# Optimization experiments

Measured on AMD Instinct MI355X. Metric: run time of the kernel, lower is better.

Reference implementation:

```python
import jax, jax.numpy as jnp
import numpy as np

BN_EPS = 1e-5

def _conv1x1(x, W, b):
    # x: [B,C,H,W], W: [O,C], b: [O]
    return jnp.einsum('bchw,oc->bohw', x, W) + b[None, :, None, None]

def setup_inputs() -> dict:
    key = jax.random.key(0)
    ks = jax.random.split(key, 9)
    B, C, H, W = 8, 256, 64, 64
    Ci = C // 2
    s_in = 0.05  # small init scale to keep softmax well-conditioned
    return {
        'x': jax.random.normal(ks[0], (B, C, H, W), jnp.float32),
        'theta_w': jax.random.normal(ks[1], (Ci, C), jnp.float32) * s_in,
        'theta_b': jnp.zeros((Ci,), jnp.float32),
        'phi_w': jax.random.normal(ks[2], (Ci, C), jnp.float32) * s_in,
        'phi_b': jnp.zeros((Ci,), jnp.float32),
        'g_w': jax.random.normal(ks[3], (Ci, C), jnp.float32) * s_in,
        'g_b': jnp.zeros((Ci,), jnp.float32),
        'out_w': jax.random.normal(ks[4], (C, Ci), jnp.float32) * s_in,
        'out_b': jnp.zeros((C,), jnp.float32),
        'gamma': jnp.ones((C,), jnp.float32),
        'beta': jnp.zeros((C,), jnp.float32),
    }

def reference(x, theta_w, theta_b, phi_w, phi_b, g_w, g_b, out_w, out_b, gamma, beta):
    B, C, H, W = x.shape
    Ci = C // 2
    N = H * W
    theta = _conv1x1(x, theta_w, theta_b).reshape(B, Ci, N)  # [B,Ci,N]
    phi = _conv1x1(x, phi_w, phi_b).reshape(B, Ci, N)        # [B,Ci,N]
    g = _conv1x1(x, g_w, g_b).reshape(B, Ci, N)              # [B,Ci,N]
    scale = 1.0 / jnp.sqrt(jnp.asarray(Ci, x.dtype))
    sim = jnp.einsum('bcn,bcm->bnm', theta, phi) * scale     # [B,N,N]
    attn = jax.nn.softmax(sim, axis=-1)
    y = jnp.einsum('bnm,bcm->bcn', attn, g).reshape(B, Ci, H, W)
    y = _conv1x1(y, out_w, out_b)                            # [B,C,H,W]
    # BatchNorm2d, training-mode statistics (biased variance), as in torch default
    mean = y.mean(axis=(0, 2, 3))
    var = y.var(axis=(0, 2, 3))
    y = (y - mean[None, :, None, None]) * jax.lax.rsqrt(var + BN_EPS)[None, :, None, None]
    y = y * gamma[None, :, None, None] + beta[None, :, None, None]
    return x + y
```

## Files before the change

### kernel.cpp

```cpp
#include <hip/hip_runtime.h>
#include <hip/hip_bf16.h>

typedef __bf16 bf16x8 __attribute__((ext_vector_type(8)));
typedef float f32x4 __attribute__((ext_vector_type(4)));
typedef float f32x16 __attribute__((ext_vector_type(16)));

#define B_ 8
#define C_ 256
#define CI 128
#define N_ 4096

__device__ __forceinline__ float exp2fast(float x) {
    return __builtin_amdgcn_exp2f(x);
}
__device__ __forceinline__ ushort f2bf(float f) {
    union { float f; unsigned u; } v; v.f = f;
    unsigned r = v.u + 0x7fffu + ((v.u >> 16) & 1u);
    return (ushort)(r >> 16);
}
__device__ __forceinline__ float bf2f(ushort u) {
    union { unsigned u; float f; } v; v.u = ((unsigned)u) << 16;
    return v.f;
}
__device__ __forceinline__ unsigned cvtpk(float lo, float hi) {
    unsigned r;
    asm("v_cvt_pk_bf16_f32 %0, %1, %2" : "=v"(r) : "v"(lo), "v"(hi));
    return r;
}
__device__ __forceinline__ void plswap(unsigned& a, unsigned& b) {
    asm volatile("v_permlane32_swap_b32 %0, %1" : "+v"(a), "+v"(b));
}
__device__ __forceinline__ void gld16(const void* src, void* dst) {
    __builtin_amdgcn_global_load_lds(
        (const __attribute__((address_space(1))) unsigned*)src,
        (__attribute__((address_space(3))) unsigned*)dst, 16, 0, 0);
}

__global__ void k_prep(const float* __restrict__ tw, const float* __restrict__ pw,
                       const float* __restrict__ gw, const float* __restrict__ ow,
                       ushort* __restrict__ wbf, ushort* __restrict__ owbf) {
    int idx = blockIdx.x * 256 + threadIdx.x;
    if (idx < 384 * 256) {
        int i = idx >> 8, c = idx & 255;
        float v = (i < 128) ? tw[i * 256 + c]
                : (i < 256) ? pw[(i - 128) * 256 + c]
                            : gw[(i - 256) * 256 + c];
        wbf[idx] = f2bf(v);
    }
    if (idx < 256 * 128) owbf[idx] = f2bf(ow[idx]);
}

__global__ __launch_bounds__(256) void k_transpose(const float* __restrict__ x,
                                                   ushort* __restrict__ xt) {
    __shared__ __align__(16) float tile[64][65];
    int b = blockIdx.z, c0 = blockIdx.y * 64, n0 = blockIdx.x * 64;
    int t = threadIdx.x;
    int cl = t >> 2, nc = (t & 3) * 16;
    const float* src = x + ((size_t)(b * 256 + c0 + cl)) * N_ + n0 + nc;
#pragma unroll
    for (int j = 0; j < 4; j++) {
        float4 v = *reinterpret_cast<const float4*>(src + 4 * j);
        tile[cl][nc + 4 * j + 0] = v.x;
        tile[cl][nc + 4 * j + 1] = v.y;
        tile[cl][nc + 4 * j + 2] = v.z;
        tile[cl][nc + 4 * j + 3] = v.w;
    }
    __syncthreads();
    int nl = t >> 2, cc = (t & 3) * 16;
    ushort* dst = xt + ((size_t)b * N_ + n0 + nl) * 256 + c0 + cc;
#pragma unroll
    for (int j = 0; j < 4; j++) {
        ushort4 o;
        o.x = f2bf(tile[cc + 4 * j + 0][nl]);
        o.y = f2bf(tile[cc + 4 * j + 1][nl]);
        o.z = f2bf(tile[cc + 4 * j + 2][nl]);
        o.w = f2bf(tile[cc + 4 * j + 3][nl]);
        *reinterpret_cast<ushort4*>(dst + 4 * j) = o;
    }
}

__global__ __launch_bounds__(256) void k_qkv(const ushort* __restrict__ wbf,
                                             const ushort* __restrict__ xt,
                                             const float* __restrict__ tb,
                                             const float* __restrict__ pb,
                                             const float* __restrict__ gb,
                                             ushort* __restrict__ qt,
                                             ushort* __restrict__ kt,
                                             ushort* __restrict__ gv) {
    __shared__ __align__(16) ushort lt[4][64][72];
    int nt = blockIdx.x, it = blockIdx.y, b = blockIdx.z;
    int tid = threadIdx.x, w = tid >> 6, l = tid & 63, lr = l & 15, lg = l >> 4;
    int i_off = it * 128 + (w >> 1) * 64;
    int n_off = nt * 128 + (w & 1) * 64;
    const ushort* xb = xt + (size_t)b * N_ * 256;

    f32x4 acc[4][4];
#pragma unroll
    for (int i = 0; i < 4; i++)
#pragma unroll
        for (int j = 0; j < 4; j++) acc[i][j] = (f32x4)0.0f;

#pragma unroll
    for (int kc = 0; kc < 8; kc++) {
        int ko = kc * 32 + lg * 8;
        bf16x8 a[4], bb[4];
#pragma unroll
        for (int fi = 0; fi < 4; fi++)
            a[fi] = *reinterpret_cast<const bf16x8*>(wbf + (size_t)(i_off + fi * 16 + lr) * 256 + ko);
#pragma unroll
        for (int fn = 0; fn < 4; fn++)
            bb[fn] = *reinterpret_cast<const bf16x8*>(xb + (size_t)(n_off + fn * 16 + lr) * 256 + ko);
#pragma unroll
        for (int fi = 0; fi < 4; fi++)
#pragma unroll
            for (int fn = 0; fn < 4; fn++)
                acc[fi][fn] = __builtin_amdgcn_mfma_f32_16x16x32_bf16(a[fi], bb[fn], acc[fi][fn], 0, 0, 0);
    }

    const float* bias = (it == 0) ? tb : (it == 1) ? pb : gb;
    const float mul = (it == 0) ? (0.08838834764831845f * 1.4426950408889634f) : 1.0f;
    if (it == 2) {
        char* g = (char*)(gv + (size_t)b * CI * N_);
#pragma unroll
        for (int fi = 0; fi < 4; fi++)
#pragma unroll
            for (int reg = 0; reg < 4; reg++) {
                int cl = (w >> 1) * 64 + fi * 16 + lg * 4 + reg;
                float bv = bias[cl];
                int cbyte = (cl & 7) * 16 + (cl >> 3) * 512;
#pragma unroll
                for (int fn = 0; fn < 4; fn++) {
                    int n = n_off + fn * 16 + lr;
                    size_t byte = (size_t)(n >> 5) * 8192 + cbyte
                                + ((n >> 3) & 3) * 128 + (n & 7) * 2;
                    *(ushort*)(g + byte) = f2bf(acc[fi][fn][reg] + bv);
                }
            }
    } else {
#pragma unroll
        for (int fi = 0; fi < 4; fi++)
#pragma unroll
            for (int reg = 0; reg < 4; reg++) {
                int il = fi * 16 + lg * 4 + reg;
                float bv = bias[(w >> 1) * 64 + il];
#pragma unroll
                for (int fn = 0; fn < 4; fn++)
                    lt[w][fn * 16 + lr][il] = f2bf((acc[fi][fn][reg] + bv) * mul);
            }
        __builtin_amdgcn_s_waitcnt(0);
        ushort* dst = ((it == 0) ? qt : kt) + (size_t)b * N_ * CI;
        ushort* drow = dst + (size_t)(n_off + l) * CI + (w >> 1) * 64;
#pragma unroll
        for (int cc = 0; cc < 8; cc++) {
            uint4 v = *reinterpret_cast<uint4*>(&lt[w][l][cc * 8]);
            *reinterpret_cast<uint4*>(drow + cc * 8) = v;
        }
    }
}

__global__ __launch_bounds__(256, 2) void k_attn(const ushort* __restrict__ qt,
                                                 const ushort* __restrict__ kt,
                                                 const ushort* __restrict__ gv,
                                                 ushort* __restrict__ yt) {
    __shared__ __align__(16) char smem[65536];
    int bid = blockIdx.x;
    int b = bid & 7, qb = bid >> 3;
    int tid = threadIdx.x, w = tid >> 6, l = tid & 63;
    int p = w >> 1, s = w & 1;
    int l31 = l & 31, lh = l >> 5;
    const ushort* qtb = qt + (size_t)b * N_ * CI;
    const ushort* ktb = kt + (size_t)b * N_ * CI;
    const ushort* gvb = gv + (size_t)b * CI * N_;
    char* kbuf = smem + p * 16384;
    char* vbuf = smem + 32768 + p * 16384;
    const int pbase = p * 2048;
    const int nq = qb * 64 + s * 32;
    const int q = nq + l31;
    const int swk = (l31 & 7) << 4;
    const int vrb = (l31 & 7) * 16 + lh * 128 + (l31 >> 3) * 512;

    bf16x8 qf[8];
#pragma unroll
    for (int kc = 0; kc < 8; kc++)
        qf[kc] = *reinterpret_cast<const bf16x8*>(qtb + (size_t)q * CI + kc * 16 + lh * 8);

    f32x16 acc[4];
#pragma unroll
    for (int fc = 0; fc < 4; fc++) acc[fc] = (f32x16)0.0f;
    float lrun = 0.f;

#define STAGE(t_, bi)                                                              \
    do {                                                                           \
        int m0_ = pbase + (t_) * 32;                                               \
        const char* ks_ = (const char*)(ktb + (size_t)m0_ * CI);                   \
        const char* vs_ = (const char*)gvb + (size_t)m0_ * 256;                    \
        char* kd_ = kbuf + (bi) * 8192;                                            \
        char* vd_ = vbuf + (bi) * 8192;                                            \
        _Pragma("unroll")                                                          \
        for (int i_ = 0; i_ < 4; ++i_) {                                           \
            int cc = i_ * 128 + s * 64 + l;                                        \
            int m_ = cc >> 4, hb = (cc & 15) << 4;                                 \
            gld16(ks_ + m_ * 256 + (hb ^ ((m_ & 7) << 4)), kd_ + cc * 16);         \
        }                                                                          \
        _Pragma("unroll")                                                          \
        for (int i_ = 0; i_ < 4; ++i_) {                                           \
            int cc = i_ * 128 + s * 64 + l;                                        \
            gld16(vs_ + cc * 16, vd_ + cc * 16);                                   \
        }                                                                          \
    } while (0)

    STAGE(0, 0);
    __syncthreads();

    for (int t = 0; t < 64; ++t) {
        int cur = t & 1;
        if (t < 63) STAGE(t + 1, cur ^ 1);
        const char* kbc = kbuf + cur * 8192;
        const char* vbc = vbuf + cur * 8192;

        f32x16 Sa = (f32x16)0.0f, Sb = (f32x16)0.0f;
        __builtin_amdgcn_s_setprio(1);
#pragma unroll
        for (int kc = 0; kc < 8; kc += 2) {
            bf16x8 kf0 = *reinterpret_cast<const bf16x8*>(
                kbc + l31 * 256 + ((kc * 32 + lh * 16) ^ swk));
            bf16x8 kf1 = *reinterpret_cast<const bf16x8*>(
                kbc + l31 * 256 + (((kc + 1) * 32 + lh * 16) ^ swk));
            Sa = __builtin_amdgcn_mfma_f32_32x32x16_bf16(kf0, qf[kc], Sa, 0, 0, 0);
            Sb = __builtin_amdgcn_mfma_f32_32x32x16_bf16(kf1, qf[kc + 1], Sb, 0, 0, 0);
        }
        __builtin_amdgcn_s_setprio(0);

        float pv[16];
        float rs = 0.f;
#pragma unroll
        for (int r = 0; r < 16; r++) {
            pv[r] = exp2fast(Sa[r] + Sb[r]);
            rs += pv[r];
        }
        lrun += rs;

        unsigned u0 = cvtpk(pv[0], pv[1]),  u1 = cvtpk(pv[2], pv[3]);
        unsigned u2 = cvtpk(pv[4], pv[5]),  u3 = cvtpk(pv[6], pv[7]);
        unsigned u4 = cvtpk(pv[8], pv[9]),  u5 = cvtpk(pv[10], pv[11]);
        unsigned u6 = cvtpk(pv[12], pv[13]), u7 = cvtpk(pv[14], pv[15]);
        plswap(u0, u2);
        plswap(u1, u3);
        plswap(u4, u6);
        plswap(u5, u7);
        union { unsigned u[4]; bf16x8 v; } pb0, pb1;
        pb0.u[0] = u0; pb0.u[1] = u1; pb0.u[2] = u2; pb0.u[3] = u3;
        pb1.u[0] = u4; pb1.u[1] = u5; pb1.u[2] = u6; pb1.u[3] = u7;

        __builtin_amdgcn_s_setprio(1);
#pragma unroll
        for (int mk = 0; mk < 2; mk++) {
            bf16x8 pf = mk ? pb1.v : pb0.v;
#pragma unroll
            for (int fc = 0; fc < 4; fc++) {
                bf16x8 vf = *reinterpret_cast<const bf16x8*>(vbc + vrb + mk * 256 + fc * 2048);
                acc[fc] = __builtin_amdgcn_mfma_f32_32x32x16_bf16(vf, pf, acc[fc], 0, 0, 0);
            }
        }
        __builtin_amdgcn_s_setprio(0);
        __syncthreads();
    }
#undef STAGE

    lrun += __shfl_xor(lrun, 32);

    float* accb = (float*)smem;
    float* mlb = (float*)(smem + 34816);
    if (p == 0) {
        float* ab = accb + s * (64 * 68) + l * 68;
#pragma unroll
        for (int fc = 0; fc < 4; fc++)
            *reinterpret_cast<f32x16*>(ab + fc * 16) = acc[fc];
        if (l < 32) mlb[s * 32 + l] = lrun;
    }
    __syncthreads();
    if (p == 1) {
        float l0 = mlb[s * 32 + l31];
        float inv = 1.f / (lrun + l0);
        const float* ab = accb + s * (64 * 68) + l * 68;
        ushort* yb = yt + (size_t)b * N_ * CI + (size_t)q * CI;
#pragma unroll
        for (int fc = 0; fc < 4; fc++) {
            f32x16 a0 = *reinterpret_cast<const f32x16*>(ab + fc * 16);
#pragma unroll
            for (int rg = 0; rg < 4; rg++) {
                ushort4 o;
                o.x = f2bf((acc[fc][rg * 4 + 0] + a0[rg * 4 + 0]) * inv);
                o.y = f2bf((acc[fc][rg * 4 + 1] + a0[rg * 4 + 1]) * inv);
                o.z = f2bf((acc[fc][rg * 4 + 2] + a0[rg * 4 + 2]) * inv);
                o.w = f2bf((acc[fc][rg * 4 + 3] + a0[rg * 4 + 3]) * inv);
                *reinterpret_cast<ushort4*>(yb + fc * 32 + rg * 8 + lh * 4) = o;
            }
        }
    }
}

__global__ __launch_bounds__(256) void k_outconv(const ushort* __restrict__ owbf,
                                                 const ushort* __restrict__ yt,
                                                 const float* __restrict__ ob,
                                                 ushort* __restrict__ pre,
                                                 float* __restrict__ part) {
    int nt = blockIdx.x, ot = blockIdx.y, b = blockIdx.z;
    int tid = threadIdx.x, w = tid >> 6, l = tid & 63, lr = l & 15, lg = l >> 4;
    int o_off = ot * 128 + (w >> 1) * 64;
    int n_off = nt * 128 + (w & 1) * 64;
    const ushort* yb = yt + (size_t)b * N_ * CI;

    f32x4 acc[4][4];
#pragma unroll
    for (int i = 0; i < 4; i++)
#pragma unroll
        for (int j = 0; j < 4; j++) acc[i][j] = (f32x4)0.0f;

#pragma unroll
    for (int kc = 0; kc < 4; kc++) {
        int ko = kc * 32 + lg * 8;
        bf16x8 a[4], bb[4];
#pragma unroll
        for (int fo = 0; fo < 4; fo++)
            a[fo] = *reinterpret_cast<const bf16x8*>(owbf + (size_t)(o_off + fo * 16 + lr) * CI + ko);
#pragma unroll
        for (int fn = 0; fn < 4; fn++)
            bb[fn] = *reinterpret_cast<const bf16x8*>(yb + (size_t)(n_off + fn * 16 + lr) * CI + ko);
#pragma unroll
        for (int fo = 0; fo < 4; fo++)
#pragma unroll
            for (int fn = 0; fn < 4; fn++)
                acc[fo][fn] = __builtin_amdgcn_mfma_f32_16x16x32_bf16(a[fo], bb[fn], acc[fo][fn], 0, 0, 0);
    }

    ushort* pb_ = pre + (size_t)b * C_ * N_;
#pragma unroll
    for (int fo = 0; fo < 4; fo++)
#pragma unroll
        for (int reg = 0; reg < 4; reg++) {
            int o = o_off + fo * 16 + lg * 4 + reg;
            float bv = ob[o];
            float s1 = 0.f, s2 = 0.f;
#pragma unroll
            for (int fn = 0; fn < 4; fn++) {
                float v = acc[fo][fn][reg] + bv;
                pb_[(size_t)o * N_ + n_off + fn * 16 + lr] = f2bf(v);
                s1 += v;
                s2 += v * v;
            }
#pragma unroll
            for (int d = 1; d < 16; d <<= 1) {
                s1 += __shfl_xor(s1, d);
                s2 += __shfl_xor(s2, d);
            }
            if (lr == 0) {
                int slot = (b * 32 + nt) * 2 + (w & 1);
                part[((size_t)o * 512 + slot) * 2 + 0] = s1;
                part[((size_t)o * 512 + slot) * 2 + 1] = s2;
            }
        }
}

__global__ void k_stats(const float* __restrict__ part, const float* __restrict__ gamma,
                        const float* __restrict__ beta, float* __restrict__ stats) {
    int o = blockIdx.x, t = threadIdx.x;
    __shared__ float r1[256], r2[256];
    float s1 = part[((size_t)o * 512 + t) * 2 + 0] + part[((size_t)o * 512 + t + 256) * 2 + 0];
    float s2 = part[((size_t)o * 512 + t) * 2 + 1] + part[((size_t)o * 512 + t + 256) * 2 + 1];
    r1[t] = s1; r2[t] = s2;
    __syncthreads();
    for (int s = 128; s > 0; s >>= 1) {
        if (t < s) { r1[t] += r1[t + s]; r2[t] += r2[t + s]; }
        __syncthreads();
    }
    if (t == 0) {
        float cnt = 1.f / (float)(B_ * N_);
        float mean = r1[0] * cnt;
        float var = r2[0] * cnt - mean * mean;
        float inv = rsqrtf(var + 1e-5f);
        float a = gamma[o] * inv;
        stats[o * 2 + 0] = a;
        stats[o * 2 + 1] = beta[o] - mean * a;
    }
}

__global__ void k_final(const float* __restrict__ x, const ushort* __restrict__ pre,
                        const float* __restrict__ stats, float* __restrict__ out) {
    int idx = blockIdx.x * 256 + threadIdx.x;
    int o = (idx >> 10) & 255;
    float a = stats[o * 2 + 0], c = stats[o * 2 + 1];
    float4 xv = reinterpret_cast<const float4*>(x)[idx];
    ushort4 pv = reinterpret_cast<const ushort4*>(pre)[idx];
    float4 ov;
    ov.x = xv.x + bf2f(pv.x) * a + c;
    ov.y = xv.y + bf2f(pv.y) * a + c;
    ov.z = xv.z + bf2f(pv.z) * a + c;
    ov.w = xv.w + bf2f(pv.w) * a + c;
    reinterpret_cast<float4*>(out)[idx] = ov;
}

extern "C" void kernel_launch(void* const* d_in, const int* in_sizes, int n_in,
                              void* d_out, int out_size, void* d_ws, size_t ws_size,
                              hipStream_t stream) {
    const float* x  = (const float*)d_in[0];
    const float* tw = (const float*)d_in[1];
    const float* tb = (const float*)d_in[2];
    const float* pw = (const float*)d_in[3];
    const float* pb = (const float*)d_in[4];
    const float* gw = (const float*)d_in[5];
    const float* gb = (const float*)d_in[6];
    const float* ow = (const float*)d_in[7];
    const float* ob = (const float*)d_in[8];
    const float* gamma = (const float*)d_in[9];
    const float* beta  = (const float*)d_in[10];

    char* ws = (char*)d_ws;
    const size_t WBF_OFF  = 0;
    const size_t OWBF_OFF = WBF_OFF + 196608;
    const size_t XT_OFF   = OWBF_OFF + 65536;
    const size_t QT_OFF   = XT_OFF + 16777216;
    const size_t KT_OFF   = QT_OFF + 8388608;
    const size_t GV_OFF   = KT_OFF + 8388608;
    const size_t YT_OFF   = GV_OFF + 8388608;
    const size_t PRE_OFF  = YT_OFF + 8388608;
    const size_t PART_OFF = PRE_OFF + 16777216;
    const size_t ST_OFF   = PART_OFF + 1048576;

    ushort* wbf  = (ushort*)(ws + WBF_OFF);
    ushort* owbf = (ushort*)(ws + OWBF_OFF);
    ushort* xt   = (ushort*)(ws + XT_OFF);
    ushort* qt   = (ushort*)(ws + QT_OFF);
    ushort* kt   = (ushort*)(ws + KT_OFF);
    ushort* gv   = (ushort*)(ws + GV_OFF);
    ushort* yt   = (ushort*)(ws + YT_OFF);
    ushort* pre  = (ushort*)(ws + PRE_OFF);
    float*  part = (float*)(ws + PART_OFF);
    float*  stats= (float*)(ws + ST_OFF);

    k_prep<<<384, 256, 0, stream>>>(tw, pw, gw, ow, wbf, owbf);
    k_transpose<<<dim3(64, 4, 8), 256, 0, stream>>>(x, xt);
    k_qkv<<<dim3(32, 3, 8), 256, 0, stream>>>(wbf, xt, tb, pb, gb, qt, kt, gv);
    k_attn<<<512, 256, 0, stream>>>(qt, kt, gv, yt);
    k_outconv<<<dim3(32, 2, 8), 256, 0, stream>>>(owbf, yt, ob, pre, part);
    k_stats<<<256, 256, 0, stream>>>(part, gamma, beta, stats);
    k_final<<<8192, 256, 0, stream>>>(x, pre, stats, (float*)d_out);
}
```

Measured before the change: 168.2 us.

## Widen attention blocks to 1024 threads with four-way KV split and shared tiles

The attention kernel now runs 256 blocks of 16 waves instead of 512 blocks of 4 waves. Each block handles 128 queries with four KV partitions of 1024 keys, so each staged K/V tile is reused by four query-slice waves instead of two. The cross-partition reduction now goes through LDS in two rounds, with partition 0 summing the partials and the row sums. LDS use doubles to 128KB per block, and the higher wave count per SIMD tightens the register budget, which risks spills given the 64-float accumulators plus the Q fragments.

Measured after the change: 264.7 us. +57.4%, slower.

```diff
diff --git a/kernel.cpp b/kernel.cpp
--- a/kernel.cpp
+++ b/kernel.cpp
@@ -158,26 +158,27 @@
     }
 }
 
-__global__ __launch_bounds__(256, 2) void k_attn(const ushort* __restrict__ qt,
-                                                 const ushort* __restrict__ kt,
-                                                 const ushort* __restrict__ gv,
-                                                 ushort* __restrict__ yt) {
-    __shared__ __align__(16) char smem[65536];
+__global__ __launch_bounds__(1024, 4) void k_attn(const ushort* __restrict__ qt,
+                                                  const ushort* __restrict__ kt,
+                                                  const ushort* __restrict__ gv,
+                                                  ushort* __restrict__ yt) {
+    __shared__ __align__(16) char smem[131072];
     int bid = blockIdx.x;
     int b = bid & 7, qb = bid >> 3;
     int tid = threadIdx.x, w = tid >> 6, l = tid & 63;
-    int p = w >> 1, s = w & 1;
+    int p = w >> 2, s = w & 3;
     int l31 = l & 31, lh = l >> 5;
     const ushort* qtb = qt + (size_t)b * N_ * CI;
     const ushort* ktb = kt + (size_t)b * N_ * CI;
     const ushort* gvb = gv + (size_t)b * CI * N_;
     char* kbuf = smem + p * 16384;
-    char* vbuf = smem + 32768 + p * 16384;
-    const int pbase = p * 2048;
-    const int nq = qb * 64 + s * 32;
+    char* vbuf = smem + 65536 + p * 16384;
+    const int pbase = p * 1024;
+    const int nq = qb * 128 + s * 32;
     const int q = nq + l31;
     const int swk = (l31 & 7) << 4;
     const int vrb = (l31 & 7) * 16 + lh * 128 + (l31 >> 3) * 512;
+    const int ls = s * 64 + l;
 
     bf16x8 qf[8];
 #pragma unroll
@@ -197,14 +198,14 @@
         char* kd_ = kbuf + (bi) * 8192;                                            \
         char* vd_ = vbuf + (bi) * 8192;                                            \
         _Pragma("unroll")                                                          \
-        for (int i_ = 0; i_ < 4; ++i_) {                                           \
-            int cc = i_ * 128 + s * 64 + l;                                        \
+        for (int i_ = 0; i_ < 2; ++i_) {                                           \
+            int cc = i_ * 256 + ls;                                                \
             int m_ = cc >> 4, hb = (cc & 15) << 4;                                 \
             gld16(ks_ + m_ * 256 + (hb ^ ((m_ & 7) << 4)), kd_ + cc * 16);         \
         }                                                                          \
         _Pragma("unroll")                                                          \
-        for (int i_ = 0; i_ < 4; ++i_) {                                           \
-            int cc = i_ * 128 + s * 64 + l;                                        \
+        for (int i_ = 0; i_ < 2; ++i_) {                                           \
+            int cc = i_ * 256 + ls;                                                \
             gld16(vs_ + cc * 16, vd_ + cc * 16);                                   \
         }                                                                          \
     } while (0)
@@ -212,9 +213,9 @@
     STAGE(0, 0);
     __syncthreads();
 
-    for (int t = 0; t < 64; ++t) {
+    for (int t = 0; t < 32; ++t) {
         int cur = t & 1;
-        if (t < 63) STAGE(t + 1, cur ^ 1);
+        if (t < 31) STAGE(t + 1, cur ^ 1);
         const char* kbc = kbuf + cur * 8192;
         const char* vbc = vbuf + cur * 8192;
 
@@ -269,34 +270,47 @@
 
     lrun += __shfl_xor(lrun, 32);
 
-    float* accb = (float*)smem;
-    float* mlb = (float*)(smem + 34816);
-    if (p == 0) {
-        float* ab = accb + s * (64 * 68) + l * 68;
-#pragma unroll
-        for (int fc = 0; fc < 4; fc++)
-            *reinterpret_cast<f32x16*>(ab + fc * 16) = acc[fc];
-        if (l < 32) mlb[s * 32 + l] = lrun;
-    }
+    float* pub = (float*)smem;
+    float* mlb = (float*)(smem + 98304);
     __syncthreads();
-    if (p == 1) {
-        float l0 = mlb[s * 32 + l31];
-        float inv = 1.f / (lrun + l0);
-        const float* ab = accb + s * (64 * 68) + l * 68;
-        ushort* yb = yt + (size_t)b * N_ * CI + (size_t)q * CI;
-#pragma unroll
-        for (int fc = 0; fc < 4; fc++) {
-            f32x16 a0 = *reinterpret_cast<const f32x16*>(ab + fc * 16);
-#pragma unroll
-            for (int rg = 0; rg < 4; rg++) {
-                ushort4 o;
-                o.x = f2bf((acc[fc][rg * 4 + 0] + a0[rg * 4 + 0]) * inv);
-                o.y = f2bf((acc[fc][rg * 4 + 1] + a0[rg * 4 + 1]) * inv);
-                o.z = f2bf((acc[fc][rg * 4 + 2] + a0[rg * 4 + 2]) * inv);
-                o.w = f2bf((acc[fc][rg * 4 + 3] + a0[rg * 4 + 3]) * inv);
-                *reinterpret_cast<ushort4*>(yb + fc * 32 + rg * 8 + lh * 4) = o;
-            }
-        }
+    if (p > 0 && lh == 0) mlb[((p - 1) * 4 + s) * 32 + l31] = lrun;
+    float inv = 0.f;
+    ushort* yb = yt + ((size_t)b * N_ + q) * CI;
+#pragma unroll
+    for (int r = 0; r < 2; ++r) {
+        if (p > 0) {
+            float* base = pub + (size_t)(((p - 1) * 4 + s) * 64 + l) * 32;
+            *reinterpret_cast<f32x16*>(base)      = acc[2 * r];
+            *reinterpret_cast<f32x16*>(base + 16) = acc[2 * r + 1];
+        }
+        __syncthreads();
+        if (p == 0) {
+            if (r == 0) {
+                float tot = lrun;
+#pragma unroll
+                for (int j = 0; j < 3; ++j) tot += mlb[(j * 4 + s) * 32 + l31];
+                inv = 1.f / tot;
+            }
+#pragma unroll
+            for (int h = 0; h < 2; ++h) {
+                int fc = 2 * r + h;
+                f32x16 sum = acc[fc];
+#pragma unroll
+                for (int j = 0; j < 3; ++j)
+                    sum += *reinterpret_cast<const f32x16*>(
+                        pub + (size_t)((j * 4 + s) * 64 + l) * 32 + h * 16);
+#pragma unroll
+                for (int rg = 0; rg < 4; rg++) {
+                    ushort4 o;
+                    o.x = f2bf(sum[rg * 4 + 0] * inv);
+                    o.y = f2bf(sum[rg * 4 + 1] * inv);
+                    o.z = f2bf(sum[rg * 4 + 2] * inv);
+                    o.w = f2bf(sum[rg * 4 + 3] * inv);
+                    *reinterpret_cast<ushort4*>(yb + fc * 32 + rg * 8 + lh * 4) = o;
+                }
+            }
+        }
+        __syncthreads();
     }
 }
 
@@ -441,7 +455,7 @@
     k_prep<<<384, 256, 0, stream>>>(tw, pw, gw, ow, wbf, owbf);
     k_transpose<<<dim3(64, 4, 8), 256, 0, stream>>>(x, xt);
     k_qkv<<<dim3(32, 3, 8), 256, 0, stream>>>(wbf, xt, tb, pb, gb, qt, kt, gv);
-    k_attn<<<512, 256, 0, stream>>>(qt, kt, gv, yt);
+    k_attn<<<256, 1024, 0, stream>>>(qt, kt, gv, yt);
     k_outconv<<<dim3(32, 2, 8), 256, 0, stream>>>(owbf, yt, ob, pre, part);
     k_stats<<<256, 256, 0, stream>>>(part, gamma, beta, stats);
     k_final<<<8192, 256, 0, stream>>>(x, pre, stats, (float*)d_out);
```

## Process two query tiles per warp in attention to reuse K/V fragments

Applied to the files above, without the earlier changes.

Each warp now computes 64 query rows instead of 32, reusing every K and V fragment loaded from LDS for two MFMAs, and the grid is halved to 256 blocks. This cuts LDS read traffic and staging per unit of work. The cost is doubled accumulator registers, a larger shared-memory reduction buffer and occupancy reduced to one block per CU, leaving less latency hiding.

New measurement: 167.6 us. About the same (-0.3%).

```diff
diff --git a/kernel.cpp b/kernel.cpp
--- a/kernel.cpp
+++ b/kernel.cpp
@@ -158,11 +158,11 @@
     }
 }
 
-__global__ __launch_bounds__(256, 2) void k_attn(const ushort* __restrict__ qt,
+__global__ __launch_bounds__(256, 1) void k_attn(const ushort* __restrict__ qt,
                                                  const ushort* __restrict__ kt,
                                                  const ushort* __restrict__ gv,
                                                  ushort* __restrict__ yt) {
-    __shared__ __align__(16) char smem[65536];
+    __shared__ __align__(16) char smem[69632];
     int bid = blockIdx.x;
     int b = bid & 7, qb = bid >> 3;
     int tid = threadIdx.x, w = tid >> 6, l = tid & 63;
@@ -174,20 +174,22 @@
     char* kbuf = smem + p * 16384;
     char* vbuf = smem + 32768 + p * 16384;
     const int pbase = p * 2048;
-    const int nq = qb * 64 + s * 32;
-    const int q = nq + l31;
+    const int nq = qb * 128 + s * 64;
+    const int q0 = nq + l31, q1 = nq + 32 + l31;
     const int swk = (l31 & 7) << 4;
     const int vrb = (l31 & 7) * 16 + lh * 128 + (l31 >> 3) * 512;
 
-    bf16x8 qf[8];
-#pragma unroll
-    for (int kc = 0; kc < 8; kc++)
-        qf[kc] = *reinterpret_cast<const bf16x8*>(qtb + (size_t)q * CI + kc * 16 + lh * 8);
-
-    f32x16 acc[4];
-#pragma unroll
-    for (int fc = 0; fc < 4; fc++) acc[fc] = (f32x16)0.0f;
-    float lrun = 0.f;
+    bf16x8 qf0[8], qf1[8];
+#pragma unroll
+    for (int kc = 0; kc < 8; kc++) {
+        qf0[kc] = *reinterpret_cast<const bf16x8*>(qtb + (size_t)q0 * CI + kc * 16 + lh * 8);
+        qf1[kc] = *reinterpret_cast<const bf16x8*>(qtb + (size_t)q1 * CI + kc * 16 + lh * 8);
+    }
+
+    f32x16 acc0[4], acc1[4];
+#pragma unroll
+    for (int fc = 0; fc < 4; fc++) { acc0[fc] = (f32x16)0.0f; acc1[fc] = (f32x16)0.0f; }
+    float lr0 = 0.f, lr1 = 0.f;
 
 #define STAGE(t_, bi)                                                              \
     do {                                                                           \
@@ -218,48 +220,57 @@
         const char* kbc = kbuf + cur * 8192;
         const char* vbc = vbuf + cur * 8192;
 
-        f32x16 Sa = (f32x16)0.0f, Sb = (f32x16)0.0f;
+        f32x16 S0 = (f32x16)0.0f, S1 = (f32x16)0.0f;
         __builtin_amdgcn_s_setprio(1);
 #pragma unroll
-        for (int kc = 0; kc < 8; kc += 2) {
-            bf16x8 kf0 = *reinterpret_cast<const bf16x8*>(
+        for (int kc = 0; kc < 8; kc++) {
+            bf16x8 kf = *reinterpret_cast<const bf16x8*>(
                 kbc + l31 * 256 + ((kc * 32 + lh * 16) ^ swk));
-            bf16x8 kf1 = *reinterpret_cast<const bf16x8*>(
-                kbc + l31 * 256 + (((kc + 1) * 32 + lh * 16) ^ swk));
-            Sa = __builtin_amdgcn_mfma_f32_32x32x16_bf16(kf0, qf[kc], Sa, 0, 0, 0);
-            Sb = __builtin_amdgcn_mfma_f32_32x32x16_bf16(kf1, qf[kc + 1], Sb, 0, 0, 0);
+            S0 = __builtin_amdgcn_mfma_f32_32x32x16_bf16(kf, qf0[kc], S0, 0, 0, 0);
+            S1 = __builtin_amdgcn_mfma_f32_32x32x16_bf16(kf, qf1[kc], S1, 0, 0, 0);
         }
         __builtin_amdgcn_s_setprio(0);
 
-        float pv[16];
-        float rs = 0.f;
-#pragma unroll
-        for (int r = 0; r < 16; r++) {
-            pv[r] = exp2fast(Sa[r] + Sb[r]);
-            rs += pv[r];
-        }
-        lrun += rs;
-
-        unsigned u0 = cvtpk(pv[0], pv[1]),  u1 = cvtpk(pv[2], pv[3]);
-        unsigned u2 = cvtpk(pv[4], pv[5]),  u3 = cvtpk(pv[6], pv[7]);
-        unsigned u4 = cvtpk(pv[8], pv[9]),  u5 = cvtpk(pv[10], pv[11]);
-        unsigned u6 = cvtpk(pv[12], pv[13]), u7 = cvtpk(pv[14], pv[15]);
-        plswap(u0, u2);
-        plswap(u1, u3);
-        plswap(u4, u6);
-        plswap(u5, u7);
-        union { unsigned u[4]; bf16x8 v; } pb0, pb1;
-        pb0.u[0] = u0; pb0.u[1] = u1; pb0.u[2] = u2; pb0.u[3] = u3;
-        pb1.u[0] = u4; pb1.u[1] = u5; pb1.u[2] = u6; pb1.u[3] = u7;
+        union { unsigned u[4]; bf16x8 v; } p00, p01, p10, p11;
+        {
+            float pv[16];
+            float rs = 0.f;
+#pragma unroll
+            for (int r = 0; r < 16; r++) { pv[r] = exp2fast(S0[r]); rs += pv[r]; }
+            lr0 += rs;
+            unsigned u0 = cvtpk(pv[0], pv[1]),  u1 = cvtpk(pv[2], pv[3]);
+            unsigned u2 = cvtpk(pv[4], pv[5]),  u3 = cvtpk(pv[6], pv[7]);
+            unsigned u4 = cvtpk(pv[8], pv[9]),  u5 = cvtpk(pv[10], pv[11]);
+            unsigned u6 = cvtpk(pv[12], pv[13]), u7 = cvtpk(pv[14], pv[15]);
+            plswap(u0, u2); plswap(u1, u3); plswap(u4, u6); plswap(u5, u7);
+            p00.u[0] = u0; p00.u[1] = u1; p00.u[2] = u2; p00.u[3] = u3;
+            p01.u[0] = u4; p01.u[1] = u5; p01.u[2] = u6; p01.u[3] = u7;
+        }
+        {
+            float pv[16];
+            float rs = 0.f;
+#pragma unroll
+            for (int r = 0; r < 16; r++) { pv[r] = exp2fast(S1[r]); rs += pv[r]; }
+            lr1 += rs;
+            unsigned u0 = cvtpk(pv[0], pv[1]),  u1 = cvtpk(pv[2], pv[3]);
+            unsigned u2 = cvtpk(pv[4], pv[5]),  u3 = cvtpk(pv[6], pv[7]);
+            unsigned u4 = cvtpk(pv[8], pv[9]),  u5 = cvtpk(pv[10], pv[11]);
+            unsigned u6 = cvtpk(pv[12], pv[13]), u7 = cvtpk(pv[14], pv[15]);
+            plswap(u0, u2); plswap(u1, u3); plswap(u4, u6); plswap(u5, u7);
+            p10.u[0] = u0; p10.u[1] = u1; p10.u[2] = u2; p10.u[3] = u3;
+            p11.u[0] = u4; p11.u[1] = u5; p11.u[2] = u6; p11.u[3] = u7;
+        }
 
         __builtin_amdgcn_s_setprio(1);
 #pragma unroll
         for (int mk = 0; mk < 2; mk++) {
-            bf16x8 pf = mk ? pb1.v : pb0.v;
+            bf16x8 pf0 = mk ? p01.v : p00.v;
+            bf16x8 pf1 = mk ? p11.v : p10.v;
 #pragma unroll
             for (int fc = 0; fc < 4; fc++) {
                 bf16x8 vf = *reinterpret_cast<const bf16x8*>(vbc + vrb + mk * 256 + fc * 2048);
-                acc[fc] = __builtin_amdgcn_mfma_f32_32x32x16_bf16(vf, pf, acc[fc], 0, 0, 0);
+                acc0[fc] = __builtin_amdgcn_mfma_f32_32x32x16_bf16(vf, pf0, acc0[fc], 0, 0, 0);
+                acc1[fc] = __builtin_amdgcn_mfma_f32_32x32x16_bf16(vf, pf1, acc1[fc], 0, 0, 0);
             }
         }
         __builtin_amdgcn_s_setprio(0);
@@ -267,34 +278,49 @@
     }
 #undef STAGE
 
-    lrun += __shfl_xor(lrun, 32);
-
-    float* accb = (float*)smem;
-    float* mlb = (float*)(smem + 34816);
+    lr0 += __shfl_xor(lr0, 32);
+    lr1 += __shfl_xor(lr1, 32);
+
+    float* pub = (float*)smem;
+    float* mlb = (float*)(smem + 67584);
+    __syncthreads();
     if (p == 0) {
-        float* ab = accb + s * (64 * 68) + l * 68;
-#pragma unroll
-        for (int fc = 0; fc < 4; fc++)
-            *reinterpret_cast<f32x16*>(ab + fc * 16) = acc[fc];
-        if (l < 32) mlb[s * 32 + l] = lrun;
+        float* ab = pub + (size_t)(s * 64 + l) * 132;
+#pragma unroll
+        for (int fc = 0; fc < 4; fc++) {
+            *reinterpret_cast<f32x16*>(ab + fc * 16) = acc0[fc];
+            *reinterpret_cast<f32x16*>(ab + 64 + fc * 16) = acc1[fc];
+        }
+        if (lh == 0) {
+            mlb[s * 64 + l31] = lr0;
+            mlb[s * 64 + 32 + l31] = lr1;
+        }
     }
     __syncthreads();
     if (p == 1) {
-        float l0 = mlb[s * 32 + l31];
-        float inv = 1.f / (lrun + l0);
-        const float* ab = accb + s * (64 * 68) + l * 68;
-        ushort* yb = yt + (size_t)b * N_ * CI + (size_t)q * CI;
+        float inv0 = 1.f / (lr0 + mlb[s * 64 + l31]);
+        float inv1 = 1.f / (lr1 + mlb[s * 64 + 32 + l31]);
+        const float* ab = pub + (size_t)(s * 64 + l) * 132;
+        ushort* yb0 = yt + ((size_t)b * N_ + q0) * CI;
+        ushort* yb1 = yt + ((size_t)b * N_ + q1) * CI;
 #pragma unroll
         for (int fc = 0; fc < 4; fc++) {
             f32x16 a0 = *reinterpret_cast<const f32x16*>(ab + fc * 16);
+            f32x16 a1 = *reinterpret_cast<const f32x16*>(ab + 64 + fc * 16);
 #pragma unroll
             for (int rg = 0; rg < 4; rg++) {
                 ushort4 o;
-                o.x = f2bf((acc[fc][rg * 4 + 0] + a0[rg * 4 + 0]) * inv);
-                o.y = f2bf((acc[fc][rg * 4 + 1] + a0[rg * 4 + 1]) * inv);
-                o.z = f2bf((acc[fc][rg * 4 + 2] + a0[rg * 4 + 2]) * inv);
-                o.w = f2bf((acc[fc][rg * 4 + 3] + a0[rg * 4 + 3]) * inv);
-                *reinterpret_cast<ushort4*>(yb + fc * 32 + rg * 8 + lh * 4) = o;
+                o.x = f2bf((acc0[fc][rg * 4 + 0] + a0[rg * 4 + 0]) * inv0);
+                o.y = f2bf((acc0[fc][rg * 4 + 1] + a0[rg * 4 + 1]) * inv0);
+                o.z = f2bf((acc0[fc][rg * 4 + 2] + a0[rg * 4 + 2]) * inv0);
+                o.w = f2bf((acc0[fc][rg * 4 + 3] + a0[rg * 4 + 3]) * inv0);
+                *reinterpret_cast<ushort4*>(yb0 + fc * 32 + rg * 8 + lh * 4) = o;
+                ushort4 o1;
+                o1.x = f2bf((acc1[fc][rg * 4 + 0] + a1[rg * 4 + 0]) * inv1);
+                o1.y = f2bf((acc1[fc][rg * 4 + 1] + a1[rg * 4 + 1]) * inv1);
+                o1.z = f2bf((acc1[fc][rg * 4 + 2] + a1[rg * 4 + 2]) * inv1);
+                o1.w = f2bf((acc1[fc][rg * 4 + 3] + a1[rg * 4 + 3]) * inv1);
+                *reinterpret_cast<ushort4*>(yb1 + fc * 32 + rg * 8 + lh * 4) = o1;
             }
         }
     }
@@ -441,7 +467,7 @@
     k_prep<<<384, 256, 0, stream>>>(tw, pw, gw, ow, wbf, owbf);
     k_transpose<<<dim3(64, 4, 8), 256, 0, stream>>>(x, xt);
     k_qkv<<<dim3(32, 3, 8), 256, 0, stream>>>(wbf, xt, tb, pb, gb, qt, kt, gv);
-    k_attn<<<512, 256, 0, stream>>>(qt, kt, gv, yt);
+    k_attn<<<256, 256, 0, stream>>>(qt, kt, gv, yt);
     k_outconv<<<dim3(32, 2, 8), 256, 0, stream>>>(owbf, yt, ob, pre, part);
     k_stats<<<256, 256, 0, stream>>>(part, gamma, beta, stats);
     k_final<<<8192, 256, 0, stream>>>(x, pre, stats, (float*)d_out);
```

## Split attention keys four ways across blocks and merge partials in separate kernel

Applied to the files above, without the earlier changes.

Replaces the two-way in-block key split of the attention kernel with a four-way split across separate blocks, each handling 128 queries and 1024 keys with half the shared memory, which allows more blocks per CU. Unnormalized partial outputs are written in bf16 to reused workspace regions along with per-row partial sums, and a new merge kernel sums them and normalizes. The aim is more parallelism and occupancy, at the cost of extra global traffic, a further launch, and added bf16 rounding of the partial results. Since no running max is used, partials can be summed directly.

Result: slower. 250.4 us (+48.9%).

```diff
diff --git a/kernel.cpp b/kernel.cpp
--- a/kernel.cpp
+++ b/kernel.cpp
@@ -158,24 +158,26 @@
     }
 }
 
-__global__ __launch_bounds__(256, 2) void k_attn(const ushort* __restrict__ qt,
-                                                 const ushort* __restrict__ kt,
-                                                 const ushort* __restrict__ gv,
-                                                 ushort* __restrict__ yt) {
-    __shared__ __align__(16) char smem[65536];
+__global__ __launch_bounds__(256, 4) void k_attn_p(const ushort* __restrict__ qt,
+                                                   const ushort* __restrict__ kt,
+                                                   const ushort* __restrict__ gv,
+                                                   ushort* __restrict__ py0,
+                                                   ushort* __restrict__ py2,
+                                                   float* __restrict__ lws) {
+    __shared__ __align__(16) char smem[32768];
     int bid = blockIdx.x;
-    int b = bid & 7, qb = bid >> 3;
+    int b = bid & 7;
+    int t2 = bid >> 3;
+    int qb = t2 & 31, pq = t2 >> 5;
     int tid = threadIdx.x, w = tid >> 6, l = tid & 63;
-    int p = w >> 1, s = w & 1;
     int l31 = l & 31, lh = l >> 5;
     const ushort* qtb = qt + (size_t)b * N_ * CI;
     const ushort* ktb = kt + (size_t)b * N_ * CI;
     const ushort* gvb = gv + (size_t)b * CI * N_;
-    char* kbuf = smem + p * 16384;
-    char* vbuf = smem + 32768 + p * 16384;
-    const int pbase = p * 2048;
-    const int nq = qb * 64 + s * 32;
-    const int q = nq + l31;
+    char* kbuf = smem;
+    char* vbuf = smem + 16384;
+    const int pbase = pq * 1024;
+    const int q = qb * 128 + w * 32 + l31;
     const int swk = (l31 & 7) << 4;
     const int vrb = (l31 & 7) * 16 + lh * 128 + (l31 >> 3) * 512;
 
@@ -197,14 +199,14 @@
         char* kd_ = kbuf + (bi) * 8192;                                            \
         char* vd_ = vbuf + (bi) * 8192;                                            \
         _Pragma("unroll")                                                          \
-        for (int i_ = 0; i_ < 4; ++i_) {                                           \
-            int cc = i_ * 128 + s * 64 + l;                                        \
+        for (int i_ = 0; i_ < 2; ++i_) {                                           \
+            int cc = i_ * 256 + tid;                                               \
             int m_ = cc >> 4, hb = (cc & 15) << 4;                                 \
             gld16(ks_ + m_ * 256 + (hb ^ ((m_ & 7) << 4)), kd_ + cc * 16);         \
         }                                                                          \
         _Pragma("unroll")                                                          \
-        for (int i_ = 0; i_ < 4; ++i_) {                                           \
-            int cc = i_ * 128 + s * 64 + l;                                        \
+        for (int i_ = 0; i_ < 2; ++i_) {                                           \
+            int cc = i_ * 256 + tid;                                               \
             gld16(vs_ + cc * 16, vd_ + cc * 16);                                   \
         }                                                                          \
     } while (0)
@@ -212,9 +214,9 @@
     STAGE(0, 0);
     __syncthreads();
 
-    for (int t = 0; t < 64; ++t) {
+    for (int t = 0; t < 32; ++t) {
         int cur = t & 1;
-        if (t < 63) STAGE(t + 1, cur ^ 1);
+        if (t < 31) STAGE(t + 1, cur ^ 1);
         const char* kbc = kbuf + cur * 8192;
         const char* vbc = vbuf + cur * 8192;
 
@@ -269,35 +271,56 @@
 
     lrun += __shfl_xor(lrun, 32);
 
-    float* accb = (float*)smem;
-    float* mlb = (float*)(smem + 34816);
-    if (p == 0) {
-        float* ab = accb + s * (64 * 68) + l * 68;
-#pragma unroll
-        for (int fc = 0; fc < 4; fc++)
-            *reinterpret_cast<f32x16*>(ab + fc * 16) = acc[fc];
-        if (l < 32) mlb[s * 32 + l] = lrun;
-    }
-    __syncthreads();
-    if (p == 1) {
-        float l0 = mlb[s * 32 + l31];
-        float inv = 1.f / (lrun + l0);
-        const float* ab = accb + s * (64 * 68) + l * 68;
-        ushort* yb = yt + (size_t)b * N_ * CI + (size_t)q * CI;
-#pragma unroll
-        for (int fc = 0; fc < 4; fc++) {
-            f32x16 a0 = *reinterpret_cast<const f32x16*>(ab + fc * 16);
-#pragma unroll
-            for (int rg = 0; rg < 4; rg++) {
-                ushort4 o;
-                o.x = f2bf((acc[fc][rg * 4 + 0] + a0[rg * 4 + 0]) * inv);
-                o.y = f2bf((acc[fc][rg * 4 + 1] + a0[rg * 4 + 1]) * inv);
-                o.z = f2bf((acc[fc][rg * 4 + 2] + a0[rg * 4 + 2]) * inv);
-                o.w = f2bf((acc[fc][rg * 4 + 3] + a0[rg * 4 + 3]) * inv);
-                *reinterpret_cast<ushort4*>(yb + fc * 32 + rg * 8 + lh * 4) = o;
-            }
-        }
-    }
+    ushort* py = (pq < 2) ? (py0 + (size_t)pq * 4194304)
+                          : (py2 + (size_t)(pq - 2) * 4194304);
+    ushort* yb = py + ((size_t)b * N_ + q) * CI;
+#pragma unroll
+    for (int fc = 0; fc < 4; fc++) {
+#pragma unroll
+        for (int rg = 0; rg < 4; rg++) {
+            ushort4 o;
+            o.x = f2bf(acc[fc][rg * 4 + 0]);
+            o.y = f2bf(acc[fc][rg * 4 + 1]);
+            o.z = f2bf(acc[fc][rg * 4 + 2]);
+            o.w = f2bf(acc[fc][rg * 4 + 3]);
+            *reinterpret_cast<ushort4*>(yb + fc * 32 + rg * 8 + lh * 4) = o;
+        }
+    }
+    if (lh == 0) lws[((size_t)pq * 8 + b) * N_ + q] = lrun;
+}
+
+__global__ __launch_bounds__(256) void k_merge(const ushort* __restrict__ py0,
+                                               const ushort* __restrict__ py2,
+                                               const float* __restrict__ lws,
+                                               ushort* __restrict__ yt) {
+    int gi = blockIdx.x * 256 + threadIdx.x;
+    int c8 = gi & 15;
+    int nn = (gi >> 4) & 4095;
+    int b = gi >> 16;
+    size_t nb = (size_t)b * N_ + nn;
+    float lt = lws[nb] + lws[8 * (size_t)N_ + nb]
+             + lws[16 * (size_t)N_ + nb] + lws[24 * (size_t)N_ + nb];
+    float inv = 1.f / lt;
+    size_t base = nb * CI + c8 * 8;
+    float s[8];
+#pragma unroll
+    for (int j = 0; j < 8; j++) s[j] = 0.f;
+#pragma unroll
+    for (int pq = 0; pq < 4; pq++) {
+        const ushort* py = (pq < 2) ? (py0 + (size_t)pq * 4194304)
+                                    : (py2 + (size_t)(pq - 2) * 4194304);
+        ushort4 lo = *reinterpret_cast<const ushort4*>(py + base);
+        ushort4 hi = *reinterpret_cast<const ushort4*>(py + base + 4);
+        s[0] += bf2f(lo.x); s[1] += bf2f(lo.y); s[2] += bf2f(lo.z); s[3] += bf2f(lo.w);
+        s[4] += bf2f(hi.x); s[5] += bf2f(hi.y); s[6] += bf2f(hi.z); s[7] += bf2f(hi.w);
+    }
+    ushort4 o0, o1;
+    o0.x = f2bf(s[0] * inv); o0.y = f2bf(s[1] * inv);
+    o0.z = f2bf(s[2] * inv); o0.w = f2bf(s[3] * inv);
+    o1.x = f2bf(s[4] * inv); o1.y = f2bf(s[5] * inv);
+    o1.z = f2bf(s[6] * inv); o1.w = f2bf(s[7] * inv);
+    *reinterpret_cast<ushort4*>(yt + base) = o0;
+    *reinterpret_cast<ushort4*>(yt + base + 4) = o1;
 }
 
 __global__ __launch_bounds__(256) void k_outconv(const ushort* __restrict__ owbf,
@@ -437,11 +460,15 @@
     ushort* pre  = (ushort*)(ws + PRE_OFF);
     float*  part = (float*)(ws + PART_OFF);
     float*  stats= (float*)(ws + ST_OFF);
+    ushort* py0  = (ushort*)(ws + XT_OFF);
+    ushort* py2  = (ushort*)(ws + PRE_OFF);
+    float*  lws  = (float*)(ws + PART_OFF);
 
     k_prep<<<384, 256, 0, stream>>>(tw, pw, gw, ow, wbf, owbf);
     k_transpose<<<dim3(64, 4, 8), 256, 0, stream>>>(x, xt);
     k_qkv<<<dim3(32, 3, 8), 256, 0, stream>>>(wbf, xt, tb, pb, gb, qt, kt, gv);
-    k_attn<<<512, 256, 0, stream>>>(qt, kt, gv, yt);
+    k_attn_p<<<1024, 256, 0, stream>>>(qt, kt, gv, py0, py2, lws);
+    k_merge<<<2048, 256, 0, stream>>>(py0, py2, lws, yt);
     k_outconv<<<dim3(32, 2, 8), 256, 0, stream>>>(owbf, yt, ob, pre, part);
     k_stats<<<256, 256, 0, stream>>>(part, gamma, beta, stats);
     k_final<<<8192, 256, 0, stream>>>(x, pre, stats, (float*)d_out);
```
